# Performance work log

Hardware: AMD Instinct MI355X
Metric: run time of the kernel (lower is better)

The kernel has to match this reference:

```python
import jax, jax.numpy as jnp
import numpy as np

B = 32768
L = 1024            # harmonics length (from 1365 = L + L//3)
HID = 256
OUT = 1024


def setup_inputs() -> dict:
    key = jax.random.key(0)
    k1, k2, k3 = jax.random.split(key, 3)
    x = jax.random.normal(k1, (B, 1, L), dtype=jnp.float32)
    W1 = jax.random.normal(k2, (HID, 1365), dtype=jnp.float32) * 0.02
    b1 = jnp.zeros((HID,), dtype=jnp.float32)
    W2 = jax.random.normal(k3, (OUT, HID), dtype=jnp.float32) * 0.02
    b2 = jnp.zeros((OUT,), dtype=jnp.float32)
    return {"x": x, "W1": W1, "b1": b1, "W2": W2, "b2": b2}


def reference(x, W1, b1, W2, b2):
    # backbone is identity; squeeze channel dim -> harmonics_pred [B, L]
    h = x[:, 0, :]
    # multi-scale average pooling (method='average'), vectorized over batch
    s1 = h                                               # scale 1: [B, 1024]
    s2 = h[:, : (L // 2) * 2].reshape(-1, L // 2, 2).mean(axis=-1)   # [B, 512]
    s3 = h[:, : (L // 3) * 3].reshape(-1, L // 3, 3).mean(axis=-1)   # [B, 341]
    m = L // 3                                           # min_len = 341
    summed = s1[:, :m] + s2[:, :m] + s3                  # [B, 341]
    feat = jnp.concatenate([h, summed], axis=1)          # [B, 1365]
    # fund_head MLP (dropout inactive in eval)
    hid = jax.nn.relu(feat @ W1.T + b1)                  # [B, 256]
    fund = hid @ W2.T + b2                               # [B, 1024]
    return fund[:, None, :], h
```

## Files before the change

kernel.cpp:

```cpp
#include <hip/hip_runtime.h>
#include <stdint.h>
#include <stddef.h>

typedef __attribute__((ext_vector_type(8))) short short8;
typedef __attribute__((ext_vector_type(4))) short short4v;
typedef __attribute__((ext_vector_type(4))) float floatx4;

#define MFMA_BF16(A, B, C) __builtin_amdgcn_mfma_f32_16x16x32_bf16((A), (B), (C), 0, 0, 0)

static constexpr int NB   = 32768;
static constexpr int LV   = 1024;
static constexpr int HIDV = 256;
static constexpr int OUTV = 1024;
static constexpr int MSUM = 341;
static constexpr int SPAD = 384;
static constexpr int K1   = 1365;
static constexpr int K1P  = 1408;
static constexpr size_t HOFF = (size_t)NB * OUTV;

__device__ __forceinline__ short f2bf(float f) {
  union { float f; uint32_t u; } c; c.f = f;
  uint32_t u = c.u;
  u += 0x7fffu + ((u >> 16) & 1u);
  return (short)(u >> 16);
}

__global__ __launch_bounds__(256) void wconv1(const float* __restrict__ W1,
                                              short* __restrict__ w1bf) {
  int idx = blockIdx.x * 256 + threadIdx.x;
  int n = idx / K1P;
  int k = idx - n * K1P;
  float v = (k < K1) ? W1[n * K1 + k] : 0.f;
  w1bf[idx] = f2bf(v);
}

__global__ __launch_bounds__(256) void wconv2(const float* __restrict__ W2,
                                              short* __restrict__ w2bf) {
  int idx = blockIdx.x * 256 + threadIdx.x;
  w2bf[idx] = f2bf(W2[idx]);
}

__global__ __launch_bounds__(256) void prep_summed(const float* __restrict__ x,
                                                   short* __restrict__ sbf) {
  __shared__ __align__(16) float hs[8][1032];
  const int t = threadIdx.x;
  const int row0 = blockIdx.x * 8;
  #pragma unroll
  for (int i = 0; i < 8; ++i) {
    const float4 v = *reinterpret_cast<const float4*>(x + (size_t)(row0 + i) * LV + t * 4);
    *reinterpret_cast<float4*>(&hs[i][t * 4]) = v;
  }
  __syncthreads();
  #pragma unroll
  for (int i = 0; i < 12; ++i) {
    int e = i * 256 + t;
    int r = e / SPAD;
    int j = e - r * SPAD;
    float val = 0.f;
    if (j < MSUM) {
      val = hs[r][j]
          + 0.5f * (hs[r][2 * j] + hs[r][2 * j + 1])
          + (1.f / 3.f) * (hs[r][3 * j] + hs[r][3 * j + 1] + hs[r][3 * j + 2]);
    }
    sbf[(size_t)(row0 + r) * SPAD + j] = f2bf(val);
  }
}

__global__ __launch_bounds__(512, 2) void gemm_fused(
    const float* __restrict__ x, const short* __restrict__ sbf,
    const short* __restrict__ w1bf, const short* __restrict__ w2bf,
    const float* __restrict__ b1, const float* __restrict__ b2,
    float* __restrict__ out) {
  __shared__ __align__(16) short Abuf[2][64 * 72];
  __shared__ __align__(16) short Hbuf[64 * 264];

  const int tid  = threadIdx.x;
  const int wave = tid >> 6;
  const int lane = tid & 63;
  const int l15  = lane & 15;
  const int quad = lane >> 4;
  const int row0 = blockIdx.x * 64;

  const int srow = tid >> 3;
  const int sseg = tid & 7;

  float4 xa, xb;
  short8 sa;
  const floatx4 fzero = {0.f, 0.f, 0.f, 0.f};

  auto loadA = [&](int ck) {
    if (ck < 16) {
      const float4* xr = reinterpret_cast<const float4*>(x + (size_t)(row0 + srow) * LV + ck * 64);
      xa = xr[sseg];
      xb = xr[sseg + 8];
    } else {
      sa = *reinterpret_cast<const short8*>(sbf + (size_t)(row0 + srow) * SPAD + (ck - 16) * 64 + sseg * 8);
    }
  };
  auto writeA = [&](int buf, int ck) {
    short* dst = &Abuf[buf][srow * 72];
    if (ck < 16) {
      short4v p0, p1;
      p0.x = f2bf(xa.x); p0.y = f2bf(xa.y); p0.z = f2bf(xa.z); p0.w = f2bf(xa.w);
      p1.x = f2bf(xb.x); p1.y = f2bf(xb.y); p1.z = f2bf(xb.z); p1.w = f2bf(xb.w);
      *reinterpret_cast<short4v*>(dst + sseg * 4)      = p0;
      *reinterpret_cast<short4v*>(dst + sseg * 4 + 32) = p1;
      float4* hdst = reinterpret_cast<float4*>(out + HOFF + (size_t)(row0 + srow) * LV + ck * 64);
      hdst[sseg]     = xa;
      hdst[sseg + 8] = xb;
    } else {
      *reinterpret_cast<short8*>(dst + sseg * 8) = sa;
    }
  };

  short8 Breg[2][2];
  auto loadB1 = [&](int ck) {
    const int c0 = ck * 64;
    #pragma unroll
    for (int ks = 0; ks < 2; ++ks)
      #pragma unroll
      for (int ns = 0; ns < 2; ++ns)
        Breg[ks][ns] = *reinterpret_cast<const short8*>(
            w1bf + (size_t)(wave * 32 + ns * 16 + l15) * K1P + c0 + ks * 32 + quad * 8);
  };

  floatx4 acc1[4][2];
  #pragma unroll
  for (int ms = 0; ms < 4; ++ms)
    #pragma unroll
    for (int ns = 0; ns < 2; ++ns)
      acc1[ms][ns] = fzero;

  loadA(0);
  loadB1(0);

  #pragma unroll 1
  for (int ck = 0; ck < 22; ++ck) {
    const int buf = ck & 1;
    writeA(buf, ck);
    if (ck < 21) loadA(ck + 1);
    __syncthreads();
    #pragma unroll
    for (int ks = 0; ks < 2; ++ks) {
      short8 afr[4];
      #pragma unroll
      for (int ms = 0; ms < 4; ++ms)
        afr[ms] = *reinterpret_cast<const short8*>(&Abuf[buf][(ms * 16 + l15) * 72 + ks * 32 + quad * 8]);
      #pragma unroll
      for (int ms = 0; ms < 4; ++ms)
        #pragma unroll
        for (int ns = 0; ns < 2; ++ns)
          acc1[ms][ns] = MFMA_BF16(afr[ms], Breg[ks][ns], acc1[ms][ns]);
    }
    if (ck < 21) loadB1(ck + 1);
  }

  #pragma unroll
  for (int ms = 0; ms < 4; ++ms) {
    #pragma unroll
    for (int ns = 0; ns < 2; ++ns) {
      const int n = wave * 32 + ns * 16 + l15;
      const float bias = b1[n];
      #pragma unroll
      for (int r = 0; r < 4; ++r) {
        const int m = ms * 16 + quad * 4 + r;
        float v = acc1[ms][ns][r] + bias;
        Hbuf[m * 264 + n] = f2bf(v > 0.f ? v : 0.f);
      }
    }
  }
  __syncthreads();

  short8 B2[4];
  auto loadB2 = [&](int half, int kc) {
    #pragma unroll
    for (int ns = 0; ns < 4; ++ns)
      B2[ns] = *reinterpret_cast<const short8*>(
          w2bf + (size_t)(half * 512 + wave * 64 + ns * 16 + l15) * HIDV + kc * 32 + quad * 8);
  };

  #pragma unroll 1
  for (int half = 0; half < 2; ++half) {
    floatx4 acc2[4][4];
    #pragma unroll
    for (int ms = 0; ms < 4; ++ms)
      #pragma unroll
      for (int ns = 0; ns < 4; ++ns)
        acc2[ms][ns] = fzero;
    loadB2(half, 0);
    #pragma unroll 1
    for (int kc = 0; kc < 8; ++kc) {
      short8 afr[4];
      #pragma unroll
      for (int ms = 0; ms < 4; ++ms)
        afr[ms] = *reinterpret_cast<const short8*>(&Hbuf[(ms * 16 + l15) * 264 + kc * 32 + quad * 8]);
      short8 bc[4];
      #pragma unroll
      for (int ns = 0; ns < 4; ++ns) bc[ns] = B2[ns];
      if (kc < 7) loadB2(half, kc + 1);
      #pragma unroll
      for (int ms = 0; ms < 4; ++ms)
        #pragma unroll
        for (int ns = 0; ns < 4; ++ns)
          acc2[ms][ns] = MFMA_BF16(afr[ms], bc[ns], acc2[ms][ns]);
    }
    #pragma unroll
    for (int ms = 0; ms < 4; ++ms) {
      #pragma unroll
      for (int ns = 0; ns < 4; ++ns) {
        const int o = half * 512 + wave * 64 + ns * 16 + l15;
        const float bias = b2[o];
        #pragma unroll
        for (int r = 0; r < 4; ++r) {
          const int m = ms * 16 + quad * 4 + r;
          out[(size_t)(row0 + m) * OUTV + o] = acc2[ms][ns][r] + bias;
        }
      }
    }
  }
}

extern "C" void kernel_launch(void* const* d_in, const int* in_sizes, int n_in,
                              void* d_out, int out_size, void* d_ws, size_t ws_size,
                              hipStream_t stream) {
  const float* x  = (const float*)d_in[0];
  const float* W1 = (const float*)d_in[1];
  const float* b1 = (const float*)d_in[2];
  const float* W2 = (const float*)d_in[3];
  const float* b2 = (const float*)d_in[4];
  float* out = (float*)d_out;

  char* ws = (char*)d_ws;
  short* sbf  = (short*)(ws);
  short* w1bf = (short*)(ws + 25165824);
  short* w2bf = (short*)(ws + 25165824 + 720896);

  hipLaunchKernelGGL(wconv1, dim3(1408), dim3(256), 0, stream, W1, w1bf);
  hipLaunchKernelGGL(wconv2, dim3(1024), dim3(256), 0, stream, W2, w2bf);
  hipLaunchKernelGGL(prep_summed, dim3(NB / 8), dim3(256), 0, stream, x, sbf);
  hipLaunchKernelGGL(gemm_fused, dim3(NB / 64), dim3(512), 0, stream,
                     x, sbf, w1bf, w2bf, b1, b2, out);
}
```

Measured before the change: 475.7 us.

## Fold pooling into effective W1 and drop summed-feature prep kernel

Since the pooled features are linear in h, the pooling weights are folded into an effective 256x1024 W1 (W1[:, :1024] plus scaled contributions from the summed columns). This removes the prep_summed kernel, its workspace round-trip and 6 of the 22 K-chunks of the first GEMM. It also double-buffers B1 fragments into registers, splits the second GEMM into quarters with fewer accumulators, and raises launch bounds occupancy to 4 blocks. Folding before bf16 rounding changes numerics slightly.

```diff
diff --git a/kernel.cpp b/kernel.cpp
--- a/kernel.cpp
+++ b/kernel.cpp
@@ -3,7 +3,6 @@
 #include <stddef.h>
 
 typedef __attribute__((ext_vector_type(8))) short short8;
-typedef __attribute__((ext_vector_type(4))) short short4v;
 typedef __attribute__((ext_vector_type(4))) float floatx4;
 
 #define MFMA_BF16(A, B, C) __builtin_amdgcn_mfma_f32_16x16x32_bf16((A), (B), (C), 0, 0, 0)
@@ -12,10 +11,6 @@
 static constexpr int LV   = 1024;
 static constexpr int HIDV = 256;
 static constexpr int OUTV = 1024;
-static constexpr int MSUM = 341;
-static constexpr int SPAD = 384;
-static constexpr int K1   = 1365;
-static constexpr int K1P  = 1408;
 static constexpr size_t HOFF = (size_t)NB * OUTV;
 
 __device__ __forceinline__ short f2bf(float f) {
@@ -25,12 +20,16 @@
   return (short)(u >> 16);
 }
 
-__global__ __launch_bounds__(256) void wconv1(const float* __restrict__ W1,
-                                              short* __restrict__ w1bf) {
+__global__ __launch_bounds__(256) void wconv1eff(const float* __restrict__ W1,
+                                                 short* __restrict__ w1bf) {
   int idx = blockIdx.x * 256 + threadIdx.x;
-  int n = idx / K1P;
-  int k = idx - n * K1P;
-  float v = (k < K1) ? W1[n * K1 + k] : 0.f;
+  int n = idx >> 10;
+  int k = idx & 1023;
+  const float* r = W1 + (size_t)n * 1365;
+  float v = r[k];
+  if (k < 341)  v += r[1024 + k];
+  if (k < 682)  v += 0.5f * r[1024 + (k >> 1)];
+  if (k < 1023) v += (1.f / 3.f) * r[1024 + k / 3];
   w1bf[idx] = f2bf(v);
 }
 
@@ -40,34 +39,8 @@
   w2bf[idx] = f2bf(W2[idx]);
 }
 
-__global__ __launch_bounds__(256) void prep_summed(const float* __restrict__ x,
-                                                   short* __restrict__ sbf) {
-  __shared__ __align__(16) float hs[8][1032];
-  const int t = threadIdx.x;
-  const int row0 = blockIdx.x * 8;
-  #pragma unroll
-  for (int i = 0; i < 8; ++i) {
-    const float4 v = *reinterpret_cast<const float4*>(x + (size_t)(row0 + i) * LV + t * 4);
-    *reinterpret_cast<float4*>(&hs[i][t * 4]) = v;
-  }
-  __syncthreads();
-  #pragma unroll
-  for (int i = 0; i < 12; ++i) {
-    int e = i * 256 + t;
-    int r = e / SPAD;
-    int j = e - r * SPAD;
-    float val = 0.f;
-    if (j < MSUM) {
-      val = hs[r][j]
-          + 0.5f * (hs[r][2 * j] + hs[r][2 * j + 1])
-          + (1.f / 3.f) * (hs[r][3 * j] + hs[r][3 * j + 1] + hs[r][3 * j + 2]);
-    }
-    sbf[(size_t)(row0 + r) * SPAD + j] = f2bf(val);
-  }
-}
-
-__global__ __launch_bounds__(512, 2) void gemm_fused(
-    const float* __restrict__ x, const short* __restrict__ sbf,
+__global__ __launch_bounds__(512, 4) void gemm_fused(
+    const float* __restrict__ x,
     const short* __restrict__ w1bf, const short* __restrict__ w2bf,
     const float* __restrict__ b1, const float* __restrict__ b2,
     float* __restrict__ out) {
@@ -85,43 +58,32 @@
   const int sseg = tid & 7;
 
   float4 xa, xb;
-  short8 sa;
   const floatx4 fzero = {0.f, 0.f, 0.f, 0.f};
 
+  const float4* xrow = reinterpret_cast<const float4*>(x + (size_t)(row0 + srow) * LV);
+  float4* hrow = reinterpret_cast<float4*>(out + HOFF + (size_t)(row0 + srow) * LV);
+
   auto loadA = [&](int ck) {
-    if (ck < 16) {
-      const float4* xr = reinterpret_cast<const float4*>(x + (size_t)(row0 + srow) * LV + ck * 64);
-      xa = xr[sseg];
-      xb = xr[sseg + 8];
-    } else {
-      sa = *reinterpret_cast<const short8*>(sbf + (size_t)(row0 + srow) * SPAD + (ck - 16) * 64 + sseg * 8);
-    }
+    xa = xrow[ck * 16 + 2 * sseg];
+    xb = xrow[ck * 16 + 2 * sseg + 1];
   };
   auto writeA = [&](int buf, int ck) {
-    short* dst = &Abuf[buf][srow * 72];
-    if (ck < 16) {
-      short4v p0, p1;
-      p0.x = f2bf(xa.x); p0.y = f2bf(xa.y); p0.z = f2bf(xa.z); p0.w = f2bf(xa.w);
-      p1.x = f2bf(xb.x); p1.y = f2bf(xb.y); p1.z = f2bf(xb.z); p1.w = f2bf(xb.w);
-      *reinterpret_cast<short4v*>(dst + sseg * 4)      = p0;
-      *reinterpret_cast<short4v*>(dst + sseg * 4 + 32) = p1;
-      float4* hdst = reinterpret_cast<float4*>(out + HOFF + (size_t)(row0 + srow) * LV + ck * 64);
-      hdst[sseg]     = xa;
-      hdst[sseg + 8] = xb;
-    } else {
-      *reinterpret_cast<short8*>(dst + sseg * 8) = sa;
-    }
-  };
-
-  short8 Breg[2][2];
-  auto loadB1 = [&](int ck) {
-    const int c0 = ck * 64;
+    short8 p;
+    p[0] = f2bf(xa.x); p[1] = f2bf(xa.y); p[2] = f2bf(xa.z); p[3] = f2bf(xa.w);
+    p[4] = f2bf(xb.x); p[5] = f2bf(xb.y); p[6] = f2bf(xb.z); p[7] = f2bf(xb.w);
+    *reinterpret_cast<short8*>(&Abuf[buf][srow * 72 + sseg * 8]) = p;
+    hrow[ck * 16 + 2 * sseg]     = xa;
+    hrow[ck * 16 + 2 * sseg + 1] = xb;
+  };
+
+  short8 Breg[4], Bnxt[4];
+  auto loadB1 = [&](int ck, short8* dst) {
     #pragma unroll
     for (int ks = 0; ks < 2; ++ks)
       #pragma unroll
       for (int ns = 0; ns < 2; ++ns)
-        Breg[ks][ns] = *reinterpret_cast<const short8*>(
-            w1bf + (size_t)(wave * 32 + ns * 16 + l15) * K1P + c0 + ks * 32 + quad * 8);
+        dst[ks * 2 + ns] = *reinterpret_cast<const short8*>(
+            w1bf + (size_t)(wave * 32 + ns * 16 + l15) * LV + ck * 64 + ks * 32 + quad * 8);
   };
 
   floatx4 acc1[4][2];
@@ -132,27 +94,29 @@
       acc1[ms][ns] = fzero;
 
   loadA(0);
-  loadB1(0);
+  loadB1(0, Breg);
 
   #pragma unroll 1
-  for (int ck = 0; ck < 22; ++ck) {
+  for (int ck = 0; ck < 16; ++ck) {
     const int buf = ck & 1;
     writeA(buf, ck);
-    if (ck < 21) loadA(ck + 1);
+    if (ck < 15) { loadA(ck + 1); loadB1(ck + 1, Bnxt); }
     __syncthreads();
     #pragma unroll
     for (int ks = 0; ks < 2; ++ks) {
       short8 afr[4];
       #pragma unroll
       for (int ms = 0; ms < 4; ++ms)
-        afr[ms] = *reinterpret_cast<const short8*>(&Abuf[buf][(ms * 16 + l15) * 72 + ks * 32 + quad * 8]);
+        afr[ms] = *reinterpret_cast<const short8*>(
+            &Abuf[buf][(ms * 16 + l15) * 72 + ks * 32 + quad * 8]);
       #pragma unroll
       for (int ms = 0; ms < 4; ++ms)
         #pragma unroll
         for (int ns = 0; ns < 2; ++ns)
-          acc1[ms][ns] = MFMA_BF16(afr[ms], Breg[ks][ns], acc1[ms][ns]);
-    }
-    if (ck < 21) loadB1(ck + 1);
+          acc1[ms][ns] = MFMA_BF16(afr[ms], Breg[ks * 2 + ns], acc1[ms][ns]);
+    }
+    #pragma unroll
+    for (int i = 0; i < 4; ++i) Breg[i] = Bnxt[i];
   }
 
   #pragma unroll
@@ -171,44 +135,44 @@
   }
   __syncthreads();
 
-  short8 B2[4];
-  auto loadB2 = [&](int half, int kc) {
-    #pragma unroll
-    for (int ns = 0; ns < 4; ++ns)
-      B2[ns] = *reinterpret_cast<const short8*>(
-          w2bf + (size_t)(half * 512 + wave * 64 + ns * 16 + l15) * HIDV + kc * 32 + quad * 8);
+  short8 B2[2], B2n[2];
+  auto loadB2 = [&](int q, int kc, short8* dst) {
+    #pragma unroll
+    for (int ns = 0; ns < 2; ++ns)
+      dst[ns] = *reinterpret_cast<const short8*>(
+          w2bf + (size_t)(q * 256 + wave * 32 + ns * 16 + l15) * HIDV + kc * 32 + quad * 8);
   };
 
   #pragma unroll 1
-  for (int half = 0; half < 2; ++half) {
-    floatx4 acc2[4][4];
+  for (int q = 0; q < 4; ++q) {
+    floatx4 acc2[4][2];
     #pragma unroll
     for (int ms = 0; ms < 4; ++ms)
       #pragma unroll
-      for (int ns = 0; ns < 4; ++ns)
+      for (int ns = 0; ns < 2; ++ns)
         acc2[ms][ns] = fzero;
-    loadB2(half, 0);
+    loadB2(q, 0, B2);
     #pragma unroll 1
     for (int kc = 0; kc < 8; ++kc) {
       short8 afr[4];
       #pragma unroll
       for (int ms = 0; ms < 4; ++ms)
-        afr[ms] = *reinterpret_cast<const short8*>(&Hbuf[(ms * 16 + l15) * 264 + kc * 32 + quad * 8]);
-      short8 bc[4];
-      #pragma unroll
-      for (int ns = 0; ns < 4; ++ns) bc[ns] = B2[ns];
-      if (kc < 7) loadB2(half, kc + 1);
+        afr[ms] = *reinterpret_cast<const short8*>(
+            &Hbuf[(ms * 16 + l15) * 264 + kc * 32 + quad * 8]);
+      if (kc < 7) loadB2(q, kc + 1, B2n);
       #pragma unroll
       for (int ms = 0; ms < 4; ++ms)
         #pragma unroll
-        for (int ns = 0; ns < 4; ++ns)
-          acc2[ms][ns] = MFMA_BF16(afr[ms], bc[ns], acc2[ms][ns]);
+        for (int ns = 0; ns < 2; ++ns)
+          acc2[ms][ns] = MFMA_BF16(afr[ms], B2[ns], acc2[ms][ns]);
+      #pragma unroll
+      for (int i = 0; i < 2; ++i) B2[i] = B2n[i];
     }
     #pragma unroll
     for (int ms = 0; ms < 4; ++ms) {
       #pragma unroll
-      for (int ns = 0; ns < 4; ++ns) {
-        const int o = half * 512 + wave * 64 + ns * 16 + l15;
+      for (int ns = 0; ns < 2; ++ns) {
+        const int o = q * 256 + wave * 32 + ns * 16 + l15;
         const float bias = b2[o];
         #pragma unroll
         for (int r = 0; r < 4; ++r) {
@@ -231,13 +195,11 @@
   float* out = (float*)d_out;
 
   char* ws = (char*)d_ws;
-  short* sbf  = (short*)(ws);
-  short* w1bf = (short*)(ws + 25165824);
-  short* w2bf = (short*)(ws + 25165824 + 720896);
-
-  hipLaunchKernelGGL(wconv1, dim3(1408), dim3(256), 0, stream, W1, w1bf);
-  hipLaunchKernelGGL(wconv2, dim3(1024), dim3(256), 0, stream, W2, w2bf);
-  hipLaunchKernelGGL(prep_summed, dim3(NB / 8), dim3(256), 0, stream, x, sbf);
+  short* w1bf = (short*)(ws);
+  short* w2bf = (short*)(ws + 524288);
+
+  hipLaunchKernelGGL(wconv1eff, dim3(1024), dim3(256), 0, stream, W1, w1bf);
+  hipLaunchKernelGGL(wconv2,    dim3(1024), dim3(256), 0, stream, W2, w2bf);
   hipLaunchKernelGGL(gemm_fused, dim3(NB / 64), dim3(512), 0, stream,
-                     x, sbf, w1bf, w2bf, b1, b2, out);
-}
+                     x, w1bf, w2bf, b1, b2, out);
+}
```

Measured after the change: 425.0 us. -10.7%, faster.
